# Performance work log

Measured on AMD Instinct MI355X. Metric: run time of the kernel, lower is better.

## Reference

```python
import jax, jax.numpy as jnp
import numpy as np

N = 2048
DIM = 1024
NH = 16
DK = DIM // NH  # 64

def setup_inputs() -> dict:
    key = jax.random.key(0)
    kx, kq, kk, kv = jax.random.split(key, 4)
    # nn.Linear(dim_in, dim_in, bias=False): init ~ U(-1/sqrt(dim_in), 1/sqrt(dim_in))
    b = 1.0 / np.sqrt(DIM)
    return {
        "x": jax.random.normal(kx, (N, DIM), dtype=jnp.float32),
        "rela": jnp.zeros((1,), dtype=jnp.float32),  # unused by the module
        "Wq": jax.random.uniform(kq, (DIM, DIM), jnp.float32, -b, b),
        "Wk": jax.random.uniform(kk, (DIM, DIM), jnp.float32, -b, b),
        "Wv": jax.random.uniform(kv, (DIM, DIM), jnp.float32, -b, b),
    }

def reference(x, rela, Wq, Wk, Wv):
    n = x.shape[0]
    scale = 1.0 / np.sqrt(DK)
    # torch Linear: x @ W.T ; reshape to [n, nh, dk] then heads first -> [nh, n, dk]
    q = (x @ Wq.T).reshape(n, NH, DK).transpose(1, 0, 2)
    k = (x @ Wk.T).reshape(n, NH, DK).transpose(1, 0, 2)
    v = (x @ Wv.T).reshape(n, NH, DK).transpose(1, 0, 2)
    dist = jnp.einsum('hnd,hmd->hnm', q, k) * scale  # [nh, n, n]
    dist = jax.nn.softmax(dist, axis=-1)
    att = jnp.einsum('hnm,hmd->hnd', dist, v)        # [nh, n, dk]
    return att.transpose(1, 0, 2).reshape(n, DIM)
```

## Files before the change

kernel.cpp:

```cpp
#include <hip/hip_runtime.h>

#define SN 2048
#define SDIM 1024
#define SNH 16
#define SDK 64

typedef short short8 __attribute__((ext_vector_type(8)));
typedef short s16x4 __attribute__((ext_vector_type(4)));
typedef unsigned short u16;
typedef u16 u16x4 __attribute__((ext_vector_type(4)));
typedef unsigned u32x4 __attribute__((ext_vector_type(4)));
typedef float f32x4 __attribute__((ext_vector_type(4)));

__device__ __forceinline__ u16 f2b(float f){
  unsigned u = __builtin_bit_cast(unsigned, f);
  u += 0x7fffu + ((u >> 16) & 1u);
  return (u16)(u >> 16);
}

__device__ __forceinline__ float b2f(u16 b){
  unsigned u = ((unsigned)b) << 16;
  return __builtin_bit_cast(float, u);
}

__device__ __forceinline__ float fast_exp2(float x){
#if __has_builtin(__builtin_amdgcn_exp2f)
  return __builtin_amdgcn_exp2f(x);
#else
  float r; asm("v_exp_f32 %0, %1" : "=v"(r) : "v"(x)); return r;
#endif
}

__device__ __forceinline__ void async_cp16(const void* g, void* l){
  __builtin_amdgcn_global_load_lds(
      (const __attribute__((address_space(1))) unsigned*)g,
      (__attribute__((address_space(3))) unsigned*)l, 16, 0, 0);
}

__global__ void conv_all(const float* __restrict__ x, const float* __restrict__ wq,
                         const float* __restrict__ wk, const float* __restrict__ wv,
                         u16* __restrict__ xb, u16* __restrict__ wb){
  const int NX4 = (SN * SDIM) / 4;
  const int NW4 = (SDIM * SDIM) / 4;
  const int total = NX4 + 3 * NW4;
  int i = blockIdx.x * blockDim.x + threadIdx.x;
  int stride = gridDim.x * blockDim.x;
  for (int idx = i; idx < total; idx += stride){
    const float* src; u16* dst; int off;
    if (idx < NX4){ src = x; dst = xb; off = idx; }
    else {
      int t = idx - NX4; int ws = t >> 18; off = t & (NW4 - 1);
      src = (ws == 0) ? wq : ((ws == 1) ? wk : wv);
      dst = wb + (size_t)ws * SDIM * SDIM;
    }
    float4 v = reinterpret_cast<const float4*>(src)[off];
    u16x4 o = { f2b(v.x), f2b(v.y), f2b(v.z), f2b(v.w) };
    *reinterpret_cast<u16x4*>(&dst[(size_t)off * 4]) = o;
  }
}

__global__ __launch_bounds__(256) void proj_gemm(const u16* __restrict__ xb, const u16* __restrict__ wb,
                                                 u16* __restrict__ qb, u16* __restrict__ kb,
                                                 u16* __restrict__ vtb){
  __shared__ __align__(16) u16 Asm[2][128 * 64];
  __shared__ __align__(16) u16 Bsm[2][128 * 64];
  const int tid = threadIdx.x, w = tid >> 6, lane = tid & 63;
  const int r = lane & 15, hi = lane >> 4;

  int flat = blockIdx.x + 16 * blockIdx.y + 128 * blockIdx.z;
  int sw = (flat & 7) * 48 + (flat >> 3);
  const int tm = (sw & 15) * 128;
  int rest = sw >> 4;
  const int tn = (rest & 7) * 128;
  const int z = rest >> 3;

  const u16* W = wb + (size_t)z * SDIM * SDIM;
  const int wr = w >> 1, wc = w & 1;
  const int srow = lane >> 3;
  const int schunk = (lane & 7) ^ (lane >> 3);
  f32x4 acc[4][4] = {};

  auto stage = [&](int b, int kt){
#pragma unroll
    for (int c = 0; c < 4; c++){
      int row = w * 32 + c * 8;
      async_cp16(xb + (size_t)(tm + row + srow) * SDIM + kt + schunk * 8, &Asm[b][row * 64]);
      async_cp16(W  + (size_t)(tn + row + srow) * SDIM + kt + schunk * 8, &Bsm[b][row * 64]);
    }
  };

  stage(0, 0);
  asm volatile("s_waitcnt vmcnt(0)" ::: "memory");
  __builtin_amdgcn_s_barrier();
  __builtin_amdgcn_sched_barrier(0);

  int cur = 0;
  for (int kt = 0; kt < SDIM; kt += 64){
    if (kt + 64 < SDIM) stage(cur ^ 1, kt + 64);
    __builtin_amdgcn_s_setprio(1);
#pragma unroll
    for (int kk = 0; kk < 2; kk++){
      short8 af[4], bf[4];
      int cc = (kk * 4 + hi) ^ (r & 7);
#pragma unroll
      for (int mr = 0; mr < 4; mr++)
        af[mr] = *reinterpret_cast<const short8*>(&Asm[cur][(wr * 64 + mr * 16 + r) * 64 + cc * 8]);
#pragma unroll
      for (int nr = 0; nr < 4; nr++)
        bf[nr] = *reinterpret_cast<const short8*>(&Bsm[cur][(wc * 64 + nr * 16 + r) * 64 + cc * 8]);
#pragma unroll
      for (int mr = 0; mr < 4; mr++)
#pragma unroll
        for (int nr = 0; nr < 4; nr++)
          acc[mr][nr] = __builtin_amdgcn_mfma_f32_16x16x32_bf16(af[mr], bf[nr], acc[mr][nr], 0, 0, 0);
    }
    __builtin_amdgcn_s_setprio(0);
    asm volatile("s_waitcnt vmcnt(0)" ::: "memory");
    __builtin_amdgcn_s_barrier();
    __builtin_amdgcn_sched_barrier(0);
    cur ^= 1;
  }

  if (z == 2){
#pragma unroll
    for (int mr = 0; mr < 4; mr++)
#pragma unroll
      for (int nr = 0; nr < 4; nr++){
        u16x4 o4 = { f2b(acc[mr][nr][0]), f2b(acc[mr][nr][1]),
                     f2b(acc[mr][nr][2]), f2b(acc[mr][nr][3]) };
        int col = tn + wc * 64 + nr * 16 + r;
        int row = tm + wr * 64 + mr * 16 + hi * 4;
        *reinterpret_cast<u16x4*>(&vtb[(size_t)col * SN + row]) = o4;
      }
  } else {
    u16* outp = (z == 0) ? qb : kb;
    const float scl = (z == 0) ? 0.18033688011112043f : 1.0f;
#pragma unroll
    for (int mr = 0; mr < 4; mr++)
#pragma unroll
      for (int nr = 0; nr < 4; nr++)
#pragma unroll
        for (int j = 0; j < 4; j++){
          int row = tm + wr * 64 + mr * 16 + hi * 4 + j;
          int col = tn + wc * 64 + nr * 16 + r;
          outp[(size_t)row * SDIM + col] = f2b(acc[mr][nr][j] * scl);
        }
  }
}

__global__ __launch_bounds__(256, 3) void attn(const u16* __restrict__ qb, const u16* __restrict__ kb,
                                               const u16* __restrict__ vtb,
                                               u16* __restrict__ po, float* __restrict__ pl){
  __shared__ __align__(16) u16 klds[2][64 * 64];
  __shared__ __align__(16) u16 vlds[2][64 * 64];
  const int tid = threadIdx.x, w = tid >> 6, lane = tid & 63;
  const int r = lane & 15, hi = lane >> 4;

  int flat = blockIdx.x + 16 * blockIdx.y + 256 * blockIdx.z;
  int sw = (flat & 7) * 128 + (flat >> 3);
  const int q0 = (sw & 15) * 128, h = (sw >> 4) & 15, z = sw >> 8;

  const int srow_off = lane >> 3;
  const int schunk   = (lane & 7) ^ (lane >> 3);

  short8 aq[2][2];
#pragma unroll
  for (int sub = 0; sub < 2; sub++){
    int qrow = q0 + w * 32 + sub * 16 + r;
    aq[sub][0] = *reinterpret_cast<const short8*>(&qb[(size_t)qrow * SDIM + h * SDK + hi * 8]);
    aq[sub][1] = *reinterpret_cast<const short8*>(&qb[(size_t)qrow * SDIM + h * SDK + 32 + hi * 8]);
  }
  f32x4 oacc[2][4] = {};
  float lacc0 = 0.f, lacc1 = 0.f;

  auto stage = [&](int b, int t){
#pragma unroll
    for (int c = 0; c < 2; c++){
      int rho = w * 16 + c * 8 + srow_off;
      int kvp = 32 * (rho >> 5) + 8 * ((rho >> 2) & 3) + 4 * ((rho >> 4) & 1) + (rho & 3);
      async_cp16(kb  + (size_t)(t + kvp) * SDIM + h * SDK + schunk * 8,
                 &klds[b][(w * 16 + c * 8) * 64]);
      int row = rho;
      async_cp16(vtb + (size_t)(h * SDK + row) * SN + t + schunk * 8,
                 &vlds[b][(w * 16 + c * 8) * 64]);
    }
  };

  const int t0 = z * (SN / 4), tend = t0 + (SN / 4);
  stage(0, t0);
  asm volatile("s_waitcnt vmcnt(0)" ::: "memory");
  __builtin_amdgcn_s_barrier();
  __builtin_amdgcn_sched_barrier(0);

  int cur = 0;
  for (int t = t0; t < tend; t += 64){
    if (t + 64 < tend) stage(cur ^ 1, t + 64);

    const u16* kbuf = &klds[cur][0];
    const u16* vbuf = &vlds[cur][0];

    f32x4 s0[4], s1[4];
    __builtin_amdgcn_s_setprio(1);
#pragma unroll
    for (int ct = 0; ct < 4; ct++){
      int row = ct * 16 + r;
      int c0 = hi ^ (r & 7);
      short8 bk0 = *reinterpret_cast<const short8*>(&kbuf[row * 64 + c0 * 8]);
      short8 bk1 = *reinterpret_cast<const short8*>(&kbuf[row * 64 + (c0 ^ 4) * 8]);
      f32x4 zero = {};
      s0[ct] = __builtin_amdgcn_mfma_f32_16x16x32_bf16(bk0, aq[0][0], zero, 0, 0, 0);
      s1[ct] = __builtin_amdgcn_mfma_f32_16x16x32_bf16(bk0, aq[1][0], zero, 0, 0, 0);
      s0[ct] = __builtin_amdgcn_mfma_f32_16x16x32_bf16(bk1, aq[0][1], s0[ct], 0, 0, 0);
      s1[ct] = __builtin_amdgcn_mfma_f32_16x16x32_bf16(bk1, aq[1][1], s1[ct], 0, 0, 0);
    }
    __builtin_amdgcn_s_setprio(0);

    uint2 pc0[4], pc1[4];
#pragma unroll
    for (int ct = 0; ct < 4; ct++){
      float a0 = fast_exp2(s0[ct][0]), a1 = fast_exp2(s0[ct][1]);
      float a2 = fast_exp2(s0[ct][2]), a3 = fast_exp2(s0[ct][3]);
      lacc0 += (a0 + a1) + (a2 + a3);
      pc0[ct].x = (__builtin_bit_cast(unsigned, a0) >> 16) |
                  (__builtin_bit_cast(unsigned, a1) & 0xffff0000u);
      pc0[ct].y = (__builtin_bit_cast(unsigned, a2) >> 16) |
                  (__builtin_bit_cast(unsigned, a3) & 0xffff0000u);
      float b0 = fast_exp2(s1[ct][0]), b1 = fast_exp2(s1[ct][1]);
      float b2 = fast_exp2(s1[ct][2]), b3 = fast_exp2(s1[ct][3]);
      lacc1 += (b0 + b1) + (b2 + b3);
      pc1[ct].x = (__builtin_bit_cast(unsigned, b0) >> 16) |
                  (__builtin_bit_cast(unsigned, b1) & 0xffff0000u);
      pc1[ct].y = (__builtin_bit_cast(unsigned, b2) >> 16) |
                  (__builtin_bit_cast(unsigned, b3) & 0xffff0000u);
    }
    short8 paf0[2], paf1[2];
#pragma unroll
    for (int c = 0; c < 2; c++){
      u32x4 u0 = { pc0[2*c].x, pc0[2*c].y, pc0[2*c+1].x, pc0[2*c+1].y };
      u32x4 u1 = { pc1[2*c].x, pc1[2*c].y, pc1[2*c+1].x, pc1[2*c+1].y };
      paf0[c] = __builtin_bit_cast(short8, u0);
      paf1[c] = __builtin_bit_cast(short8, u1);
    }

    __builtin_amdgcn_s_setprio(1);
#pragma unroll
    for (int dt = 0; dt < 4; dt++){
      int row = dt * 16 + r;
      int swz = row & 7;
      short8 bvc[2];
#pragma unroll
      for (int c = 0; c < 2; c++)
        bvc[c] = *reinterpret_cast<const short8*>(&vbuf[row * 64 + ((4 * c + hi) ^ swz) * 8]);
#pragma unroll
      for (int c = 0; c < 2; c++){
        oacc[0][dt] = __builtin_amdgcn_mfma_f32_16x16x32_bf16(paf0[c], bvc[c], oacc[0][dt], 0, 0, 0);
        oacc[1][dt] = __builtin_amdgcn_mfma_f32_16x16x32_bf16(paf1[c], bvc[c], oacc[1][dt], 0, 0, 0);
      }
    }
    __builtin_amdgcn_s_setprio(0);

    asm volatile("s_waitcnt vmcnt(0)" ::: "memory");
    __builtin_amdgcn_s_barrier();
    __builtin_amdgcn_sched_barrier(0);
    cur ^= 1;
  }

  lacc0 += __shfl_xor(lacc0, 16); lacc0 += __shfl_xor(lacc0, 32);
  lacc1 += __shfl_xor(lacc1, 16); lacc1 += __shfl_xor(lacc1, 32);

  const size_t zh = (size_t)z * SNH + h;
#pragma unroll
  for (int sub = 0; sub < 2; sub++)
#pragma unroll
    for (int dt = 0; dt < 4; dt++)
#pragma unroll
      for (int j = 0; j < 4; j++){
        int row = q0 + w * 32 + sub * 16 + hi * 4 + j;
        po[(zh * SN + row) * SDK + dt * 16 + r] = f2b(oacc[sub][dt][j]);
      }
  if (hi == 0){
    pl[zh * SN + q0 + w * 32 + r] = lacc0;
    pl[zh * SN + q0 + w * 32 + 16 + r] = lacc1;
  }
}

__global__ void merge(const u16* __restrict__ po, const float* __restrict__ pl,
                      float* __restrict__ out){
  int gid = blockIdx.x * blockDim.x + threadIdx.x;
  int c4 = gid & 15;
  int rowid = gid >> 4;
  int h = rowid & 15, q = rowid >> 4;
  float L = 0.f;
  float4 o = { 0.f, 0.f, 0.f, 0.f };
#pragma unroll
  for (int z = 0; z < 4; z++){
    size_t zh = (size_t)z * SNH + h;
    L += pl[zh * SN + q];
    u16x4 a = *reinterpret_cast<const u16x4*>(&po[(zh * SN + q) * SDK + c4 * 4]);
    o.x += b2f(a[0]); o.y += b2f(a[1]); o.z += b2f(a[2]); o.w += b2f(a[3]);
  }
  float rL = 1.0f / L;
  o.x *= rL; o.y *= rL; o.z *= rL; o.w *= rL;
  reinterpret_cast<float4*>(&out[(size_t)q * SDIM + h * SDK])[c4] = o;
}

extern "C" void kernel_launch(void* const* d_in, const int* in_sizes, int n_in,
                              void* d_out, int out_size, void* d_ws, size_t ws_size,
                              hipStream_t stream){
  const float* x  = (const float*)d_in[0];
  const float* Wq = (const float*)d_in[2];
  const float* Wk = (const float*)d_in[3];
  const float* Wv = (const float*)d_in[4];
  float* out = (float*)d_out;

  char* ws = (char*)d_ws;
  u16* xb  = (u16*)(ws);
  u16* wb  = (u16*)(ws + (4  << 20));
  u16* qb  = (u16*)(ws + (10 << 20));
  u16* kb  = (u16*)(ws + (14 << 20));
  u16* vtb = (u16*)(ws + (18 << 20));
  u16* po  = (u16*)(ws + (22 << 20));
  float* pl = (float*)(ws + (38 << 20));

  conv_all<<<2048, 256, 0, stream>>>(x, Wq, Wk, Wv, xb, wb);

  dim3 pg(SDIM / 64, SDIM / 128, 3);
  proj_gemm<<<pg, 256, 0, stream>>>(xb, wb, qb, kb, vtb);

  dim3 ag(SN / 128, SNH, 4);
  attn<<<ag, 256, 0, stream>>>(qb, kb, vtb, po, pl);

  merge<<<(SN * SNH * 16) / 256, 256, 0, stream>>>(po, pl, out);
}
```

Before: 64.42 us.

## Shrink projection GEMM tiles to 64x128 and split K across warp groups

The projection GEMM now uses 64x128 output tiles with 512 threads, so each block runs 8 waves. The waves form two groups that each handle half of every 64-wide K step, and their partial results are reduced through shared memory (reusing the B buffer) before the bf16 store. This doubles the number of blocks and raises waves per block, aiming for better occupancy and more latency hiding on the 2048x1024x3 GEMM. The cost is less data reuse per tile, an extra LDS reduction plus barrier, and the loss of the previous block-swizzle ordering for L2 locality.

```diff
diff --git a/kernel.cpp b/kernel.cpp
--- a/kernel.cpp
+++ b/kernel.cpp
@@ -59,33 +59,28 @@
   }
 }
 
-__global__ __launch_bounds__(256) void proj_gemm(const u16* __restrict__ xb, const u16* __restrict__ wb,
-                                                 u16* __restrict__ qb, u16* __restrict__ kb,
-                                                 u16* __restrict__ vtb){
-  __shared__ __align__(16) u16 Asm[2][128 * 64];
+__global__ __launch_bounds__(512, 6) void proj_gemm(const u16* __restrict__ xb, const u16* __restrict__ wb,
+                                                    u16* __restrict__ qb, u16* __restrict__ kb,
+                                                    u16* __restrict__ vtb){
+  __shared__ __align__(16) u16 Asm[2][64 * 64];
   __shared__ __align__(16) u16 Bsm[2][128 * 64];
   const int tid = threadIdx.x, w = tid >> 6, lane = tid & 63;
   const int r = lane & 15, hi = lane >> 4;
-
-  int flat = blockIdx.x + 16 * blockIdx.y + 128 * blockIdx.z;
-  int sw = (flat & 7) * 48 + (flat >> 3);
-  const int tm = (sw & 15) * 128;
-  int rest = sw >> 4;
-  const int tn = (rest & 7) * 128;
-  const int z = rest >> 3;
-
+  const int tm = blockIdx.x * 64, tn = blockIdx.y * 128;
+  const int z = blockIdx.z;
   const u16* W = wb + (size_t)z * SDIM * SDIM;
-  const int wr = w >> 1, wc = w & 1;
+  const int kk = w >> 2;
+  const int wr = (w >> 1) & 1, wc = w & 1;
   const int srow = lane >> 3;
   const int schunk = (lane & 7) ^ (lane >> 3);
-  f32x4 acc[4][4] = {};
+  f32x4 acc[2][4] = {};
 
   auto stage = [&](int b, int kt){
-#pragma unroll
-    for (int c = 0; c < 4; c++){
-      int row = w * 32 + c * 8;
-      async_cp16(xb + (size_t)(tm + row + srow) * SDIM + kt + schunk * 8, &Asm[b][row * 64]);
-      async_cp16(W  + (size_t)(tn + row + srow) * SDIM + kt + schunk * 8, &Bsm[b][row * 64]);
+    async_cp16(xb + (size_t)(tm + w * 8 + srow) * SDIM + kt + schunk * 8, &Asm[b][w * 8 * 64]);
+#pragma unroll
+    for (int c = 0; c < 2; c++){
+      int row = w * 16 + c * 8;
+      async_cp16(W + (size_t)(tn + row + srow) * SDIM + kt + schunk * 8, &Bsm[b][row * 64]);
     }
   };
 
@@ -98,18 +93,17 @@
   for (int kt = 0; kt < SDIM; kt += 64){
     if (kt + 64 < SDIM) stage(cur ^ 1, kt + 64);
     __builtin_amdgcn_s_setprio(1);
-#pragma unroll
-    for (int kk = 0; kk < 2; kk++){
-      short8 af[4], bf[4];
+    {
+      short8 af[2], bf[4];
       int cc = (kk * 4 + hi) ^ (r & 7);
 #pragma unroll
-      for (int mr = 0; mr < 4; mr++)
-        af[mr] = *reinterpret_cast<const short8*>(&Asm[cur][(wr * 64 + mr * 16 + r) * 64 + cc * 8]);
+      for (int mr = 0; mr < 2; mr++)
+        af[mr] = *reinterpret_cast<const short8*>(&Asm[cur][(wr * 32 + mr * 16 + r) * 64 + cc * 8]);
 #pragma unroll
       for (int nr = 0; nr < 4; nr++)
         bf[nr] = *reinterpret_cast<const short8*>(&Bsm[cur][(wc * 64 + nr * 16 + r) * 64 + cc * 8]);
 #pragma unroll
-      for (int mr = 0; mr < 4; mr++)
+      for (int mr = 0; mr < 2; mr++)
 #pragma unroll
         for (int nr = 0; nr < 4; nr++)
           acc[mr][nr] = __builtin_amdgcn_mfma_f32_16x16x32_bf16(af[mr], bf[nr], acc[mr][nr], 0, 0, 0);
@@ -121,30 +115,56 @@
     cur ^= 1;
   }
 
-  if (z == 2){
-#pragma unroll
-    for (int mr = 0; mr < 4; mr++)
+  float* scr = reinterpret_cast<float*>(&Bsm[0][0]);
+  const int slot = w & 3;
+  if (kk == 1){
+#pragma unroll
+    for (int mr = 0; mr < 2; mr++)
 #pragma unroll
       for (int nr = 0; nr < 4; nr++){
-        u16x4 o4 = { f2b(acc[mr][nr][0]), f2b(acc[mr][nr][1]),
-                     f2b(acc[mr][nr][2]), f2b(acc[mr][nr][3]) };
-        int col = tn + wc * 64 + nr * 16 + r;
-        int row = tm + wr * 64 + mr * 16 + hi * 4;
-        *reinterpret_cast<u16x4*>(&vtb[(size_t)col * SN + row]) = o4;
+        int fid = mr * 4 + nr;
+        int a = slot * 2048 + fid * 256 + r * 16 + ((hi + r) & 3) * 4;
+        *reinterpret_cast<f32x4*>(&scr[a]) = acc[mr][nr];
       }
-  } else {
-    u16* outp = (z == 0) ? qb : kb;
-    const float scl = (z == 0) ? 0.18033688011112043f : 1.0f;
-#pragma unroll
-    for (int mr = 0; mr < 4; mr++)
-#pragma unroll
-      for (int nr = 0; nr < 4; nr++)
-#pragma unroll
-        for (int j = 0; j < 4; j++){
-          int row = tm + wr * 64 + mr * 16 + hi * 4 + j;
+  }
+  __syncthreads();
+  if (kk == 0){
+#pragma unroll
+    for (int mr = 0; mr < 2; mr++)
+#pragma unroll
+      for (int nr = 0; nr < 4; nr++){
+        int fid = mr * 4 + nr;
+        int a = slot * 2048 + fid * 256 + r * 16 + ((hi + r) & 3) * 4;
+        f32x4 t = *reinterpret_cast<const f32x4*>(&scr[a]);
+        acc[mr][nr][0] += t[0]; acc[mr][nr][1] += t[1];
+        acc[mr][nr][2] += t[2]; acc[mr][nr][3] += t[3];
+      }
+
+    if (z == 2){
+#pragma unroll
+      for (int mr = 0; mr < 2; mr++)
+#pragma unroll
+        for (int nr = 0; nr < 4; nr++){
+          u16x4 o4 = { f2b(acc[mr][nr][0]), f2b(acc[mr][nr][1]),
+                       f2b(acc[mr][nr][2]), f2b(acc[mr][nr][3]) };
           int col = tn + wc * 64 + nr * 16 + r;
-          outp[(size_t)row * SDIM + col] = f2b(acc[mr][nr][j] * scl);
+          int row = tm + wr * 32 + mr * 16 + hi * 4;
+          *reinterpret_cast<u16x4*>(&vtb[(size_t)col * SN + row]) = o4;
         }
+    } else {
+      u16* outp = (z == 0) ? qb : kb;
+      const float scl = (z == 0) ? 0.18033688011112043f : 1.0f;
+#pragma unroll
+      for (int mr = 0; mr < 2; mr++)
+#pragma unroll
+        for (int nr = 0; nr < 4; nr++)
+#pragma unroll
+          for (int j = 0; j < 4; j++){
+            int row = tm + wr * 32 + mr * 16 + hi * 4 + j;
+            int col = tn + wc * 64 + nr * 16 + r;
+            outp[(size_t)row * SDIM + col] = f2b(acc[mr][nr][j] * scl);
+          }
+    }
   }
 }
 
@@ -324,8 +344,8 @@
 
   conv_all<<<2048, 256, 0, stream>>>(x, Wq, Wk, Wv, xb, wb);
 
-  dim3 pg(SDIM / 64, SDIM / 128, 3);
-  proj_gemm<<<pg, 256, 0, stream>>>(xb, wb, qb, kb, vtb);
+  dim3 pg(SN / 64, SDIM / 128, 3);
+  proj_gemm<<<pg, 512, 0, stream>>>(xb, wb, qb, kb, vtb);
 
   dim3 ag(SN / 128, SNH, 4);
   attn<<<ag, 256, 0, stream>>>(qb, kb, vtb, po, pl);
```

Measured after the change: 60.15 us. -6.6%, faster.
